# Kernel optimization log

Measured on AMD Instinct MI355X. Metric: run time of the kernel, lower is better.

## Reference

```python
import jax, jax.numpy as jnp
import numpy as np
from jax import lax

T = 50
THETA = 1.0 - 0.0001  # max_1 - 0.0001, max_1 = T_win/T = 1.0


def conv_t(x, w, b, pad_h):
    # x: [N, C, H, W, T]; slayer conv3d has time-kernel 1 -> conv2d per timestep.
    n, c, h, wd, t = x.shape
    xb = jnp.moveaxis(x, -1, 1).reshape(n * t, c, h, wd)
    y = lax.conv_general_dilated(xb, w, (1, 1), [(pad_h, pad_h), (0, 0)])
    y = y + b[None, :, None, None]
    o, h2, w2 = y.shape[1], y.shape[2], y.shape[3]
    return jnp.moveaxis(y.reshape(n, t, o, h2, w2), 1, -1)


def if_spikes(a):
    # catCuda.getSpikes on an input stacked T times: IF neuron with constant
    # drive a per step, soft reset (v -= theta on spike). a: [N,C,H,W].
    def step(v, _):
        v = v + a
        s = (v >= THETA).astype(a.dtype)
        return v - s * THETA, s
    _, sp = lax.scan(step, jnp.zeros_like(a), None, length=T)
    return jnp.moveaxis(sp, 0, -1)  # [N,C,H,W,T]


def setup_inputs() -> dict:
    key = jax.random.key(0)
    ks = jax.random.split(key, 6)
    def w(k, shape, scale):
        return jax.random.normal(k, shape, jnp.float32) * scale
    x = jax.random.uniform(ks[0], (256, 1, 180, 1, T), jnp.float32)
    return {
        'x': x,
        'w1': w(ks[1], (16, 1, 3, 1), 0.3), 'b1': jnp.zeros(16, jnp.float32),
        'w2': w(ks[2], (32, 16, 9, 1), 0.1), 'b2': jnp.zeros(32, jnp.float32),
        'w3': w(ks[3], (32, 32, 7, 1), 0.1), 'b3': jnp.zeros(32, jnp.float32),
        'wf': w(ks[4], (4, 32, 83, 1), 0.05), 'bf': jnp.zeros(4, jnp.float32),
    }


def reference(x, w1, b1, w2, b2, w3, b3, wf, bf):
    y = conv_t(x, w1, b1, 1)                        # [N,16,180,1,T]
    y = if_spikes(jnp.sum(y, axis=4) / T)           # rate -> spikes
    y = conv_t(y, w2, b2, 1)                        # [N,32,174,1,T]
    y = if_spikes(jnp.sum(y, axis=4) / T)
    y = 1.1 * (y[:, :, 0::2] + y[:, :, 1::2])       # slayer sum-pool (2,1), weight 1.1
    y = if_spikes(jnp.sum(y, axis=4) / T)           # [N,32,87,1,T]
    y = conv_t(y, w3, b3, 1)                        # [N,32,83,1,T]
    y = if_spikes(jnp.sum(y, axis=4) / T)
    out = jnp.einsum('nchwt,ochw->not', y, wf) + bf[None, :, None]  # dense over full spatial
    return jnp.sum(out, axis=-1) / T                # sum_spikes / T -> [N,4]
```

## Files before the change

### kernel.cpp

```cpp
#include <hip/hip_runtime.h>


#define T_STEPS 50
#define THETA   0.9999f

__device__ float g_part[256 * 8];

__device__ __forceinline__ float spike_rate(float a, const float* __restrict__ tbl) {
    constexpr float INV = 50.0f / 0.9999f;
    float t = a * INV;
    float c = fminf(fmaxf(floorf(t), 0.0f), 50.0f);
    bool risky = (t > 0.5f) && (fabsf(t - rintf(t)) < 2e-4f);
    if (__ballot(risky)) {
        float v = 0.f, cnt = 0.f;
#pragma unroll 1
        for (int k = 0; k < T_STEPS; ++k) {
            v += a;
            float s = (v >= THETA) ? 1.0f : 0.0f;
            v -= s * THETA;
            cnt += s;
        }
        c = cnt;
    }
    return tbl[(int)c];
}

__device__ __forceinline__ float spike_rate_nb(float a, const float* __restrict__ tbl) {
    constexpr float INV = 50.0f / 0.9999f;
    float t = a * INV;
    float c = fminf(fmaxf(floorf(t), 0.0f), 50.0f);
    return tbl[(int)c];
}

extern "C" __global__ void __launch_bounds__(512, 4)
catnet_split(const float* __restrict__ x,
             const float* __restrict__ w1, const float* __restrict__ b1,
             const float* __restrict__ w2, const float* __restrict__ b2,
             const float* __restrict__ w3, const float* __restrict__ b3,
             const float* __restrict__ wf)
{
    const int n    = blockIdx.x >> 1;
    const int half = blockIdx.x & 1;
    const int tid  = threadIdx.x;
    const int wave = tid >> 6;
    const int lane = tid & 63;

    const int x_lo   = half ? 80 : 0;   const int x_cnt  = half ? 100 : 104;
    const int r1_lo  = half ? 81 : 0;   const int r1_cnt = half ?  99 : 103;
    const int p_lo   = half ? 41 : 0;   const int p_cnt  = half ?  46 :  48;
    const int h_lo   = half ? 42 : 0;   const int h_cnt  = half ?  41 :  42;

    __shared__ float xbar[182];
    __shared__ float r1pe[16][92];
    __shared__ float r1po[16][92];
    __shared__ float r3p[32][89];
    __shared__ alignas(16) float r4s[32][83];
    __shared__ float ratetbl[51];
    __shared__ float part[8];

    if (tid < 16)                { r1pe[tid][0] = 0.f; }
    if (tid >= 16 && tid < 32)   { r1po[tid-16][90] = 0.f; }
    if (tid >= 32 && tid < 64)   { r3p[tid-32][0] = 0.f; r3p[tid-32][88] = 0.f; }
    if (tid == 64)               { xbar[0] = 0.f; xbar[181] = 0.f; }
    if (tid >= 128 && tid < 179) { ratetbl[tid-128] = (float)(tid-128) / 50.0f; }

    const float* xn = x + (size_t)n * (180 * 50);
    if (tid < 4 * x_cnt) {
        const int h_l = tid >> 2, q = tid & 3;
        const int h   = x_lo + h_l;
        const float2* row2 = reinterpret_cast<const float2*>(xn + h * 50);
        float s = 0.f;
        for (int k = q; k < 24; k += 4) { float2 v = row2[k]; s += v.x + v.y; }
        if (q == 0)                     { float2 v = row2[24]; s += v.x + v.y; }
        s += __shfl_xor(s, 1, 4);
        s += __shfl_xor(s, 2, 4);
        if (q == 0) xbar[h + 1] = s;
    }
    __syncthreads();

    for (int idx = tid; idx < 16 * 128; idx += 512) {
        const int c = idx >> 7, h_l = idx & 127;
        const bool act = h_l < r1_cnt;
        const int h = r1_lo + (act ? h_l : 0);
        float a = w1[c*3+0] * xbar[h] + w1[c*3+1] * xbar[h+1] + w1[c*3+2] * xbar[h+2];
        a = a / 50.0f + b1[c];
        float r = spike_rate(a, ratetbl);
        if (act) {
            int H = h + 1;
            if (H & 1) r1po[c][H >> 1] = r;
            else       r1pe[c][H >> 1] = r;
        }
    }
    __syncthreads();

    {
        const int g   = __builtin_amdgcn_readfirstlane(wave);
        const bool act = lane < p_cnt;
        const int p   = p_lo + (act ? lane : 0);
        const float* wb = w2 + g * 4 * 144;

        float a0[4], a1[4];
#pragma unroll
        for (int j = 0; j < 4; ++j) { a0[j] = b2[g*4 + j]; a1[j] = a0[j]; }

        float we[5], wo[5];
#pragma unroll
        for (int d = 0; d < 5; ++d) { we[d] = r1pe[0][p + d]; wo[d] = r1po[0][p + d]; }

#pragma unroll 1
        for (int ci = 0; ci < 16; ++ci) {
            const int cn = (ci < 15) ? ci + 1 : 15;
            float weN[5], woN[5];
#pragma unroll
            for (int d = 0; d < 5; ++d) { weN[d] = r1pe[cn][p + d]; woN[d] = r1po[cn][p + d]; }

#pragma unroll
            for (int j = 0; j < 4; ++j) {
                const float* wj = wb + j * 144 + ci * 9;
#pragma unroll
                for (int kh = 0; kh < 9; ++kh) {
                    float wv  = wj[kh];
                    float xlo = (kh & 1) ? wo[kh >> 1] : we[kh >> 1];
                    float xhi = (kh & 1) ? we[(kh + 1) >> 1] : wo[kh >> 1];
                    a0[j] += wv * xlo;
                    a1[j] += wv * xhi;
                }
            }
#pragma unroll
            for (int d = 0; d < 5; ++d) { we[d] = weN[d]; wo[d] = woN[d]; }
        }
#pragma unroll
        for (int j = 0; j < 4; ++j) {
            float r20 = spike_rate(a0[j], ratetbl);
            float r21 = spike_rate(a1[j], ratetbl);
            float r3  = spike_rate_nb(1.1f * (r20 + r21), ratetbl);
            if (act) r3p[g*4 + j][p + 1] = r3;
        }
    }
    __syncthreads();

    {
        const int gg   = __builtin_amdgcn_readfirstlane(wave);
        const int g4   = gg * 4;
        const bool act = lane < h_cnt;
        const int h0   = h_lo + lane;
        const int hr   = act ? h0 : h_lo;
        const float* wb = w3 + g4 * 224;

        float a[4];
#pragma unroll
        for (int j = 0; j < 4; ++j) a[j] = b3[g4 + j];

        float rv[7];
#pragma unroll
        for (int kh = 0; kh < 7; ++kh) rv[kh] = r3p[0][hr + kh];

#pragma unroll 1
        for (int ci = 0; ci < 32; ++ci) {
            const int cn = (ci < 31) ? ci + 1 : 31;
            float rn[7];
#pragma unroll
            for (int kh = 0; kh < 7; ++kh) rn[kh] = r3p[cn][hr + kh];

#pragma unroll
            for (int j = 0; j < 4; ++j) {
                const float* wj = wb + j * 224 + ci * 7;
#pragma unroll
                for (int kh = 0; kh < 7; ++kh)
                    a[j] += wj[kh] * rv[kh];
            }
#pragma unroll
            for (int kh = 0; kh < 7; ++kh) rv[kh] = rn[kh];
        }
#pragma unroll
        for (int j = 0; j < 4; ++j) {
            float r = spike_rate(a[j], ratetbl);
            if (act) r4s[g4 + j][h0] = r;
        }
    }
    __syncthreads();

    {
        const int o = wave >> 1, q = wave & 1;
        float acc = 0.f;
        if (lane < h_cnt) {
            const int h0 = h_lo + lane;
            const float* wo = wf + o * (32 * 83);
            for (int c = q; c < 32; c += 2)
                acc += r4s[c][h0] * wo[c * 83 + h0];
        }
#pragma unroll
        for (int off = 32; off > 0; off >>= 1)
            acc += __shfl_down(acc, off, 64);
        if (lane == 0) part[wave] = acc;
    }
    __syncthreads();
    if (tid < 4)
        g_part[n * 8 + half * 4 + tid] = part[2 * tid] + part[2 * tid + 1];
}

extern "C" __global__ void __launch_bounds__(256)
catnet_finish(const float* __restrict__ bf, float* __restrict__ out)
{
    const int i = blockIdx.x * 256 + threadIdx.x;
    if (i < 1024) {
        const int n = i >> 2, o = i & 3;
        out[i] = g_part[n * 8 + o] + g_part[n * 8 + 4 + o] + bf[o];
    }
}

extern "C" void kernel_launch(void* const* d_in, const int* in_sizes, int n_in,
                              void* d_out, int out_size, void* d_ws, size_t ws_size,
                              hipStream_t stream) {
    const float* x  = (const float*)d_in[0];
    const float* w1 = (const float*)d_in[1];
    const float* b1 = (const float*)d_in[2];
    const float* w2 = (const float*)d_in[3];
    const float* b2 = (const float*)d_in[4];
    const float* w3 = (const float*)d_in[5];
    const float* b3 = (const float*)d_in[6];
    const float* wf = (const float*)d_in[7];
    const float* bf = (const float*)d_in[8];
    float* outp = (float*)d_out;

    catnet_split<<<dim3(512), dim3(512), 0, stream>>>(
        x, w1, b1, w2, b2, w3, b3, wf);
    catnet_finish<<<dim3(4), dim3(256), 0, stream>>>(bf, outp);
}
```

Baseline: 107.4 us.

## Split each sample across four blocks and pair lanes per output channel

Each sample is now split spatially into four quarter-blocks instead of two, which doubles the grid to 1024 blocks and raises the launch-bounds occupancy hint to 8. Inside the conv2 and conv3 stages, adjacent lanes now split the four output channels of a wave into two pairs. This lets a half-sized spatial tile still use most lanes while cutting per-thread accumulators and registers. The finish kernel sums four partials per sample. In exchange, halo recomputation of the xbar and r1 stages grows, and each block does more redundant setup for less useful work.

```diff
diff --git a/kernel.cpp b/kernel.cpp
--- a/kernel.cpp
+++ b/kernel.cpp
@@ -4,7 +4,7 @@
 #define T_STEPS 50
 #define THETA   0.9999f
 
-__device__ float g_part[256 * 8];
+__device__ float g_part[256 * 16];
 
 __device__ __forceinline__ float spike_rate(float a, const float* __restrict__ tbl) {
     constexpr float INV = 50.0f / 0.9999f;
@@ -32,23 +32,27 @@
     return tbl[(int)c];
 }
 
-extern "C" __global__ void __launch_bounds__(512, 4)
+extern "C" __global__ void __launch_bounds__(512, 8)
 catnet_split(const float* __restrict__ x,
              const float* __restrict__ w1, const float* __restrict__ b1,
              const float* __restrict__ w2, const float* __restrict__ b2,
              const float* __restrict__ w3, const float* __restrict__ b3,
              const float* __restrict__ wf)
 {
-    const int n    = blockIdx.x >> 1;
-    const int half = blockIdx.x & 1;
+    const int n    = blockIdx.x >> 2;
+    const int qt   = blockIdx.x & 3;
     const int tid  = threadIdx.x;
     const int wave = tid >> 6;
     const int lane = tid & 63;
 
-    const int x_lo   = half ? 80 : 0;   const int x_cnt  = half ? 100 : 104;
-    const int r1_lo  = half ? 81 : 0;   const int r1_cnt = half ?  99 : 103;
-    const int p_lo   = half ? 41 : 0;   const int p_cnt  = half ?  46 :  48;
-    const int h_lo   = half ? 42 : 0;   const int h_cnt  = half ?  41 :  42;
+    const int h_lo_t[4]  = {0, 21, 42, 63},  h_cnt_t[4]  = {21, 21, 21, 20};
+    const int p_lo_t[4]  = {0, 20, 41, 62},  p_cnt_t[4]  = {27, 28, 28, 25};
+    const int r1_lo_t[4] = {0, 39, 81, 123}, r1_cnt_t[4] = {62, 65, 65, 57};
+    const int x_lo_t[4]  = {0, 38, 80, 122}, x_cnt_t[4]  = {63, 67, 67, 58};
+    const int h_lo  = h_lo_t[qt],  h_cnt  = h_cnt_t[qt];
+    const int p_lo  = p_lo_t[qt],  p_cnt  = p_cnt_t[qt];
+    const int r1_lo = r1_lo_t[qt], r1_cnt = r1_cnt_t[qt];
+    const int x_lo  = x_lo_t[qt],  x_cnt  = x_cnt_t[qt];
 
     __shared__ float xbar[182];
     __shared__ float r1pe[16][92];
@@ -95,13 +99,15 @@
 
     {
         const int g   = __builtin_amdgcn_readfirstlane(wave);
-        const bool act = lane < p_cnt;
-        const int p   = p_lo + (act ? lane : 0);
-        const float* wb = w2 + g * 4 * 144;
-
-        float a0[4], a1[4];
-#pragma unroll
-        for (int j = 0; j < 4; ++j) { a0[j] = b2[g*4 + j]; a1[j] = a0[j]; }
+        const int jj  = lane & 1;
+        const int pl  = lane >> 1;
+        const bool act = pl < p_cnt;
+        const int p   = p_lo + (act ? pl : 0);
+        const float* wb = w2 + (g * 4 + jj * 2) * 144;
+
+        float a0[2], a1[2];
+#pragma unroll
+        for (int j = 0; j < 2; ++j) { a0[j] = b2[g*4 + jj*2 + j]; a1[j] = a0[j]; }
 
         float we[5], wo[5];
 #pragma unroll
@@ -115,7 +121,7 @@
             for (int d = 0; d < 5; ++d) { weN[d] = r1pe[cn][p + d]; woN[d] = r1po[cn][p + d]; }
 
 #pragma unroll
-            for (int j = 0; j < 4; ++j) {
+            for (int j = 0; j < 2; ++j) {
                 const float* wj = wb + j * 144 + ci * 9;
 #pragma unroll
                 for (int kh = 0; kh < 9; ++kh) {
@@ -130,40 +136,40 @@
             for (int d = 0; d < 5; ++d) { we[d] = weN[d]; wo[d] = woN[d]; }
         }
 #pragma unroll
-        for (int j = 0; j < 4; ++j) {
+        for (int j = 0; j < 2; ++j) {
             float r20 = spike_rate(a0[j], ratetbl);
             float r21 = spike_rate(a1[j], ratetbl);
             float r3  = spike_rate_nb(1.1f * (r20 + r21), ratetbl);
-            if (act) r3p[g*4 + j][p + 1] = r3;
+            if (act) r3p[g*4 + jj*2 + j][p + 1] = r3;
         }
     }
     __syncthreads();
 
     {
         const int gg   = __builtin_amdgcn_readfirstlane(wave);
-        const int g4   = gg * 4;
-        const bool act = lane < h_cnt;
-        const int h0   = h_lo + lane;
-        const int hr   = act ? h0 : h_lo;
-        const float* wb = w3 + g4 * 224;
-
-        float a[4];
-#pragma unroll
-        for (int j = 0; j < 4; ++j) a[j] = b3[g4 + j];
+        const int jj   = lane & 1;
+        const int hl   = lane >> 1;
+        const bool act = hl < h_cnt;
+        const int h0   = h_lo + (act ? hl : 0);
+        const float* wb = w3 + (gg * 4 + jj * 2) * 224;
+
+        float a[2];
+#pragma unroll
+        for (int j = 0; j < 2; ++j) a[j] = b3[gg*4 + jj*2 + j];
 
         float rv[7];
 #pragma unroll
-        for (int kh = 0; kh < 7; ++kh) rv[kh] = r3p[0][hr + kh];
+        for (int kh = 0; kh < 7; ++kh) rv[kh] = r3p[0][h0 + kh];
 
 #pragma unroll 1
         for (int ci = 0; ci < 32; ++ci) {
             const int cn = (ci < 31) ? ci + 1 : 31;
             float rn[7];
 #pragma unroll
-            for (int kh = 0; kh < 7; ++kh) rn[kh] = r3p[cn][hr + kh];
-
-#pragma unroll
-            for (int j = 0; j < 4; ++j) {
+            for (int kh = 0; kh < 7; ++kh) rn[kh] = r3p[cn][h0 + kh];
+
+#pragma unroll
+            for (int j = 0; j < 2; ++j) {
                 const float* wj = wb + j * 224 + ci * 7;
 #pragma unroll
                 for (int kh = 0; kh < 7; ++kh)
@@ -173,9 +179,9 @@
             for (int kh = 0; kh < 7; ++kh) rv[kh] = rn[kh];
         }
 #pragma unroll
-        for (int j = 0; j < 4; ++j) {
+        for (int j = 0; j < 2; ++j) {
             float r = spike_rate(a[j], ratetbl);
-            if (act) r4s[g4 + j][h0] = r;
+            if (act) r4s[gg*4 + jj*2 + j][h0] = r;
         }
     }
     __syncthreads();
@@ -196,7 +202,7 @@
     }
     __syncthreads();
     if (tid < 4)
-        g_part[n * 8 + half * 4 + tid] = part[2 * tid] + part[2 * tid + 1];
+        g_part[n * 16 + qt * 4 + tid] = part[2 * tid] + part[2 * tid + 1];
 }
 
 extern "C" __global__ void __launch_bounds__(256)
@@ -205,7 +211,8 @@
     const int i = blockIdx.x * 256 + threadIdx.x;
     if (i < 1024) {
         const int n = i >> 2, o = i & 3;
-        out[i] = g_part[n * 8 + o] + g_part[n * 8 + 4 + o] + bf[o];
+        out[i] = g_part[n * 16 + o]     + g_part[n * 16 + 4 + o]
+               + g_part[n * 16 + 8 + o] + g_part[n * 16 + 12 + o] + bf[o];
     }
 }
 
@@ -223,7 +230,7 @@
     const float* bf = (const float*)d_in[8];
     float* outp = (float*)d_out;
 
-    catnet_split<<<dim3(512), dim3(512), 0, stream>>>(
+    catnet_split<<<dim3(1024), dim3(512), 0, stream>>>(
         x, w1, b1, w2, b2, w3, b3, wf);
     catnet_finish<<<dim3(4), dim3(256), 0, stream>>>(bf, outp);
 }
```

Measured after the change: 176.5 us. +64.3%, slower.
